# Kernel tuning notes

Hardware: AMD Instinct MI355X
Metric: run time of the kernel (lower is better)

The kernel has to match this reference:

```python
import jax, jax.numpy as jnp
import numpy as np

B, S, HID = 2, 2048, 2048
H, KV, D = 32, 8, 64
GROUPS = H // KV
THETA = 10000.0
SCALE = D ** -0.5
NEG = -1e9


def setup_inputs() -> dict:
    key = jax.random.key(0)
    ks = jax.random.split(key, 5)
    x = jax.random.normal(ks[0], (B, S, 2 * HID), dtype=jnp.float32)
    # Linear weights stored as [in, out] (torch stores [out, in]; y = x @ W.T there)
    Wq = jax.random.normal(ks[1], (2 * HID, H * D), dtype=jnp.float32) * 0.02
    Wk = jax.random.normal(ks[2], (2 * HID, KV * D), dtype=jnp.float32) * 0.02
    Wv = jax.random.normal(ks[3], (2 * HID, KV * D), dtype=jnp.float32) * 0.02
    Wo = jax.random.normal(ks[4], (H * D, HID), dtype=jnp.float32) * 0.02
    # additive causal mask, broadcastable to [B, 1, S, S]
    causal = jnp.tril(jnp.ones((S, S), dtype=bool))
    attention_mask = jnp.where(causal, 0.0, NEG)[None, None].astype(jnp.float32)
    position_ids = jnp.broadcast_to(jnp.arange(S, dtype=jnp.int32)[None, :], (B, S))
    return {"combined_states": x, "attention_mask": attention_mask,
            "position_ids": position_ids, "Wq": Wq, "Wk": Wk, "Wv": Wv, "Wo": Wo}


def _rotate_half(x):
    x1, x2 = jnp.split(x, 2, axis=-1)
    return jnp.concatenate([-x2, x1], axis=-1)


def _rope_cos_sin(position_ids, dtype):
    inv_freq = 1.0 / (THETA ** (jnp.arange(0, D, 2, dtype=jnp.float32) / D))  # [D/2]
    freqs = position_ids.astype(jnp.float32)[..., None] * inv_freq  # [B, S, D/2]
    emb = jnp.concatenate([freqs, freqs], axis=-1)  # [B, S, D]
    return jnp.cos(emb).astype(dtype), jnp.sin(emb).astype(dtype)


def reference(combined_states, attention_mask, position_ids, Wq, Wk, Wv, Wo):
    x = combined_states
    q = (x @ Wq).reshape(B, S, H, D).transpose(0, 2, 1, 3)    # [B, H, S, D]
    k = (x @ Wk).reshape(B, S, KV, D).transpose(0, 2, 1, 3)   # [B, KV, S, D]
    v = (x @ Wv).reshape(B, S, KV, D).transpose(0, 2, 1, 3)
    cos, sin = _rope_cos_sin(position_ids, x.dtype)           # [B, S, D]
    cos, sin = cos[:, None], sin[:, None]                     # [B, 1, S, D]
    q = q * cos + _rotate_half(q) * sin
    k = k * cos + _rotate_half(k) * sin
    k = jnp.repeat(k, GROUPS, axis=1)                         # [B, H, S, D]
    v = jnp.repeat(v, GROUPS, axis=1)
    scores = jnp.einsum('bhqd,bhkd->bhqk', q, k) * SCALE + attention_mask
    probs = jax.nn.softmax(scores.astype(jnp.float32), axis=-1).astype(q.dtype)
    attn = jnp.einsum('bhqk,bhkd->bhqd', probs, v)            # [B, H, S, D]
    attn = attn.transpose(0, 2, 1, 3).reshape(B, S, H * D)
    return attn @ Wo
```

## Files before the change

kernel.cpp:

```cpp
#include <hip/hip_runtime.h>

#define S_LEN 2048
#define BATCH 2
#define HEADS 32
#define KVH   8
#define DH    64

typedef unsigned short u16;
typedef u16   u16x8 __attribute__((ext_vector_type(8)));
typedef u16   u16x4 __attribute__((ext_vector_type(4)));
typedef short s16x8 __attribute__((ext_vector_type(8)));
typedef float f32x4 __attribute__((ext_vector_type(4)));

__device__ __forceinline__ u16 f2bf(float f) {
    unsigned x; __builtin_memcpy(&x, &f, 4);
    x += 0x7fffu + ((x >> 16) & 1u);
    return (u16)(x >> 16);
}
__device__ __forceinline__ u16 f2bf_trunc(float f) {
    unsigned x; __builtin_memcpy(&x, &f, 4);
    return (u16)(x >> 16);
}
__device__ __forceinline__ float bf2f(u16 u) {
    unsigned x = ((unsigned)u) << 16; float f; __builtin_memcpy(&f, &x, 4); return f;
}
__device__ __forceinline__ float fexp2(float x) {
#if __has_builtin(__builtin_amdgcn_exp2f)
    return __builtin_amdgcn_exp2f(x);
#else
    return exp2f(x);
#endif
}
__device__ __forceinline__ void gll16(const void* g, void* l) {
    __builtin_amdgcn_global_load_lds((const __attribute__((address_space(1))) unsigned*)g,
                                     (__attribute__((address_space(3))) unsigned*)l, 16, 0, 0);
}

__global__ __launch_bounds__(256) void k_f32_to_bf16(const float* __restrict__ src,
                                                     u16* __restrict__ dst, int n4) {
    int i = blockIdx.x * 256 + threadIdx.x;
    if (i < n4) {
        f32x4 v = ((const f32x4*)src)[i];
        u16x4 o;
        o.x = f2bf(v.x); o.y = f2bf(v.y); o.z = f2bf(v.z); o.w = f2bf(v.w);
        ((u16x4*)dst)[i] = o;
    }
}

__global__ __launch_bounds__(256) void k_transpose_bf16(const float* __restrict__ src,
                                                        u16* __restrict__ dst,
                                                        int srcCols, int dstStride, int dstRowOff) {
    __shared__ float t[32][33];
    int r0 = blockIdx.x * 32, c0 = blockIdx.y * 32;
    int tx = threadIdx.x & 31, ty = threadIdx.x >> 5;
#pragma unroll
    for (int i = 0; i < 4; ++i)
        t[ty + 8 * i][tx] = src[(size_t)(r0 + ty + 8 * i) * srcCols + (c0 + tx)];
    __syncthreads();
#pragma unroll
    for (int i = 0; i < 4; ++i)
        dst[(size_t)(dstRowOff + c0 + ty + 8 * i) * dstStride + (r0 + tx)] = f2bf(t[tx][ty + 8 * i]);
}

template <int OUT_BF16>
__global__ __launch_bounds__(256) void k_gemm_bt(const u16* __restrict__ A,
                                                 const u16* __restrict__ Bt,
                                                 void* __restrict__ Cout,
                                                 int M, int N, int K) {
    __shared__ __align__(16) u16 As[8192];
    __shared__ __align__(16) u16 Bs[8192];
    int tid = threadIdx.x;
    int wave = tid >> 6, lane = tid & 63, m15 = lane & 15, quad = lane >> 4;
    int wm = (wave >> 1) * 64, wn = (wave & 1) * 64;
    int m0 = blockIdx.y * 128, n0 = blockIdx.x * 128;

    f32x4 acc[4][4];
#pragma unroll
    for (int i = 0; i < 4; ++i)
#pragma unroll
        for (int j = 0; j < 4; ++j) acc[i][j] = (f32x4){0.f, 0.f, 0.f, 0.f};

    int rl8 = lane >> 3;
    int sg8 = ((lane & 7) ^ rl8) * 8;
    const u16* Ag = A  + (size_t)(m0 + wave * 32 + rl8) * K + sg8;
    const u16* Bg = Bt + (size_t)(n0 + wave * 32 + rl8) * K + sg8;
    u16* Asl = As + (wave * 32) * 64;
    u16* Bsl = Bs + (wave * 32) * 64;
    int swq = m15 & 7;

    for (int k0 = 0; k0 < K; k0 += 64) {
        __syncthreads();
#pragma unroll
        for (int i = 0; i < 4; ++i) {
            gll16(Ag + (size_t)(8 * i) * K, Asl + (8 * i) * 64);
            gll16(Bg + (size_t)(8 * i) * K, Bsl + (8 * i) * 64);
        }
        Ag += 64; Bg += 64;
        __syncthreads();

#pragma unroll
        for (int kk = 0; kk < 2; ++kk) {
            int sgr = ((kk * 4 + quad) ^ swq) * 8;
            s16x8 af[4], bfr[4];
#pragma unroll
            for (int mt = 0; mt < 4; ++mt)
                af[mt] = *(const s16x8*)&As[(wm + mt * 16 + m15) * 64 + sgr];
#pragma unroll
            for (int nt = 0; nt < 4; ++nt)
                bfr[nt] = *(const s16x8*)&Bs[(wn + nt * 16 + m15) * 64 + sgr];
#pragma unroll
            for (int mt = 0; mt < 4; ++mt)
#pragma unroll
                for (int nt = 0; nt < 4; ++nt)
                    acc[mt][nt] = __builtin_amdgcn_mfma_f32_16x16x32_bf16(af[mt], bfr[nt], acc[mt][nt], 0, 0, 0);
        }
    }

#pragma unroll
    for (int mt = 0; mt < 4; ++mt)
#pragma unroll
        for (int nt = 0; nt < 4; ++nt)
#pragma unroll
            for (int r = 0; r < 4; ++r) {
                size_t row = m0 + wm + mt * 16 + quad * 4 + r;
                size_t col = n0 + wn + nt * 16 + m15;
                float v = acc[mt][nt][r];
                if (OUT_BF16) ((u16*)Cout)[row * N + col] = f2bf(v);
                else          ((float*)Cout)[row * N + col] = v;
            }
}

__global__ __launch_bounds__(256) void k_vtrans(const u16* __restrict__ qkv, u16* __restrict__ vt) {
    __shared__ u16 t[64][72];
    int s0 = blockIdx.x * 64;
    int bkv = blockIdx.y;
    int tid = threadIdx.x;
    int row = tid >> 2, seg = tid & 3;
    int b = bkv >> 3, kv = bkv & 7;
    const u16* src = qkv + (size_t)(b * S_LEN + s0 + row) * 3072 + 2560 + kv * 64 + seg * 16;
    *(u16x8*)&t[row][seg * 16]     = *(const u16x8*)(src);
    *(u16x8*)&t[row][seg * 16 + 8] = *(const u16x8*)(src + 8);
    __syncthreads();
    int d = tid >> 2, sseg = tid & 3;
    u16x8 o0, o1;
#pragma unroll
    for (int j = 0; j < 8; ++j) { o0[j] = t[sseg * 16 + j][d]; o1[j] = t[sseg * 16 + 8 + j][d]; }
    u16* dst = vt + ((size_t)bkv * 64 + d) * S_LEN + s0 + sseg * 16;
    *(u16x8*)(dst)     = o0;
    *(u16x8*)(dst + 8) = o1;
}

__global__ __launch_bounds__(256) void k_rope(const u16* __restrict__ qkv,
                                              const int* __restrict__ pos_ids,
                                              u16* __restrict__ qo, u16* __restrict__ ko) {
    int bs = blockIdx.x;
    int b = bs >> 11, s = bs & 2047;
    int tid = threadIdx.x;
    float pos = (float)pos_ids[bs];
    const u16* row = qkv + (size_t)bs * 3072;

#pragma unroll
    for (int p = tid; p < 1024; p += 256) {
        int h = p >> 5, i = p & 31;
        float inv = fexp2((float)i * -0.4152410119f);
        float ang = pos * inv;
        float sn, c; __sincosf(ang, &sn, &c);
        float a = bf2f(row[h * 64 + i]);
        float bq = bf2f(row[h * 64 + i + 32]);
        size_t base = ((size_t)(b * HEADS + h) * S_LEN + s) * DH;
        qo[base + i]      = f2bf(a * c - bq * sn);
        qo[base + i + 32] = f2bf(bq * c + a * sn);
    }
    {
        int p = tid;
        if (p < 256) {
            int kv = p >> 5, i = p & 31;
            float inv = fexp2((float)i * -0.4152410119f);
            float ang = pos * inv;
            float sn, c; __sincosf(ang, &sn, &c);
            float a = bf2f(row[2048 + kv * 64 + i]);
            float bk = bf2f(row[2048 + kv * 64 + i + 32]);
            size_t base = ((size_t)(b * KVH + kv) * S_LEN + s) * DH;
            ko[base + i]      = f2bf(a * c - bk * sn);
            ko[base + i + 32] = f2bf(bk * c + a * sn);
        }
    }
}

__global__ __launch_bounds__(256) void k_attn(const u16* __restrict__ q, const u16* __restrict__ k,
                                              const u16* __restrict__ vt, u16* __restrict__ out) {
    __shared__ __align__(16) u16 Qs[4096];
    __shared__ __align__(16) u16 Ks[4096];
    __shared__ __align__(16) u16 Vts[4096];
    __shared__ __align__(16) u16 Ps[4 * 16 * 72];
    int bh = blockIdx.y;
    int b = bh >> 5, h = bh & 31, kvh = h >> 2;
    int tid = threadIdx.x, wave = tid >> 6, lane = tid & 63, m15 = lane & 15, quad = lane >> 4;

    const u16* qhb = q + (size_t)(b * HEADS + h) * S_LEN * DH;
    const u16* kb  = k + (size_t)(b * KVH + kvh) * S_LEN * DH;
    const u16* vb  = vt + (size_t)(b * KVH + kvh) * DH * S_LEN;
    u16* PsW = &Ps[wave * 16 * 72];
    const float C = 0.1803368801f;

    int rl8 = lane >> 3;
    int sg8 = ((lane & 7) ^ rl8) * 8;
    int swq = m15 & 7;

    for (int half = 0; half < 2; ++half) {
        int jt = half ? (31 - (int)blockIdx.x) : (int)blockIdx.x;
        int q0 = jt * 64;
        __syncthreads();
        {
            const u16* qg = qhb + (size_t)(q0 + wave * 16 + rl8) * DH + sg8;
            gll16(qg,          Qs + (wave * 16) * 64);
            gll16(qg + 8 * DH, Qs + (wave * 16 + 8) * 64);
        }

        float lsum[4];
        f32x4 oacc[4];
#pragma unroll
        for (int r = 0; r < 4; ++r) lsum[r] = 0.f;
#pragma unroll
        for (int dt = 0; dt < 4; ++dt) oacc[dt] = (f32x4){0.f, 0.f, 0.f, 0.f};

        for (int ib = 0; ib <= jt; ++ib) {
            int kk0 = ib * 64;
            __syncthreads();
            {
                const u16* kg = kb + (size_t)(kk0 + wave * 16 + rl8) * DH + sg8;
                gll16(kg,          Ks + (wave * 16) * 64);
                gll16(kg + 8 * DH, Ks + (wave * 16 + 8) * 64);
                const u16* vg = vb + (size_t)(wave * 16 + rl8) * S_LEN + kk0 + sg8;
                gll16(vg,             Vts + (wave * 16) * 64);
                gll16(vg + 8 * S_LEN, Vts + (wave * 16 + 8) * 64);
            }
            __syncthreads();

            f32x4 sacc[4];
#pragma unroll
            for (int nt = 0; nt < 4; ++nt) sacc[nt] = (f32x4){0.f, 0.f, 0.f, 0.f};
#pragma unroll
            for (int kk = 0; kk < 2; ++kk) {
                int sgr = ((kk * 4 + quad) ^ swq) * 8;
                s16x8 aF = *(const s16x8*)&Qs[(wave * 16 + m15) * 64 + sgr];
#pragma unroll
                for (int nt = 0; nt < 4; ++nt) {
                    s16x8 bF = *(const s16x8*)&Ks[(nt * 16 + m15) * 64 + sgr];
                    sacc[nt] = __builtin_amdgcn_mfma_f32_16x16x32_bf16(aF, bF, sacc[nt], 0, 0, 0);
                }
            }

            bool diag = (ib == jt);
#pragma unroll
            for (int r = 0; r < 4; ++r) {
                int qrow = q0 + wave * 16 + quad * 4 + r;
#pragma unroll
                for (int nt = 0; nt < 4; ++nt) {
                    float s2 = sacc[nt][r] * C - 12.0f;
                    if (diag && (kk0 + nt * 16 + m15 > qrow)) s2 = -1e30f;
                    float p = fexp2(s2);
                    lsum[r] += p;
                    PsW[(quad * 4 + r) * 72 + nt * 16 + m15] = f2bf_trunc(p);
                }
            }

#pragma unroll
            for (int kk = 0; kk < 2; ++kk) {
                s16x8 aF = *(const s16x8*)&PsW[m15 * 72 + kk * 32 + quad * 8];
                int sgr = ((kk * 4 + quad) ^ swq) * 8;
#pragma unroll
                for (int dt = 0; dt < 4; ++dt) {
                    s16x8 bF = *(const s16x8*)&Vts[(dt * 16 + m15) * 64 + sgr];
                    oacc[dt] = __builtin_amdgcn_mfma_f32_16x16x32_bf16(aF, bF, oacc[dt], 0, 0, 0);
                }
            }
        }

#pragma unroll
        for (int r = 0; r < 4; ++r) {
            float ls = lsum[r];
#pragma unroll
            for (int off = 1; off < 16; off <<= 1) ls += __shfl_xor(ls, off, 64);
            float inv = 1.f / ls;
            int qrow = q0 + wave * 16 + quad * 4 + r;
#pragma unroll
            for (int dt = 0; dt < 4; ++dt)
                out[((size_t)(b * S_LEN) + qrow) * (size_t)(HEADS * DH) + h * DH + dt * 16 + m15] =
                    f2bf(oacc[dt][r] * inv);
        }
    }
}

extern "C" void kernel_launch(void* const* d_in, const int* in_sizes, int n_in,
                              void* d_out, int out_size, void* d_ws, size_t ws_size,
                              hipStream_t stream) {
    const float* x  = (const float*)d_in[0];
    const int*   pos = (const int*)d_in[2];
    const float* Wq = (const float*)d_in[3];
    const float* Wk = (const float*)d_in[4];
    const float* Wv = (const float*)d_in[5];
    const float* Wo = (const float*)d_in[6];

    char* ws = (char*)d_ws;
    const size_t NEED = 92274688;
    if (ws_size < NEED) return;

    u16* xbf   = (u16*)(ws);
    u16* vt    = (u16*)(ws + 16777216);
    u16* wqkvt = (u16*)(ws + 33554432);
    u16* wot   = (u16*)(ws + 58720256);
    u16* qkv   = (u16*)(ws + 67108864);
    u16* qro   = wqkvt;
    u16* kro   = qro + 8388608;
    u16* attn  = xbf;

    k_f32_to_bf16<<<16384, 256, 0, stream>>>(x, xbf, 4194304);
    {
        dim3 gq(128, 64); k_transpose_bf16<<<gq, 256, 0, stream>>>(Wq, wqkvt, 2048, 4096, 0);
        dim3 gk(128, 16); k_transpose_bf16<<<gk, 256, 0, stream>>>(Wk, wqkvt, 512, 4096, 2048);
        k_transpose_bf16<<<gk, 256, 0, stream>>>(Wv, wqkvt, 512, 4096, 2560);
        dim3 go(64, 64);  k_transpose_bf16<<<go, 256, 0, stream>>>(Wo, wot, 2048, 2048, 0);
    }
    { dim3 g(24, 32); k_gemm_bt<1><<<g, 256, 0, stream>>>(xbf, wqkvt, qkv, 4096, 3072, 4096); }
    { dim3 g(32, 16); k_vtrans<<<g, 256, 0, stream>>>(qkv, vt); }
    k_rope<<<4096, 256, 0, stream>>>(qkv, pos, qro, kro);
    { dim3 g(16, 64); k_attn<<<g, 256, 0, stream>>>(qro, kro, vt, attn); }
    { dim3 g(16, 32); k_gemm_bt<0><<<g, 256, 0, stream>>>(attn, wot, (float*)d_out, 4096, 2048, 2048); }
}
```

Before: 426.9 us.

## Process two KV tiles per attention barrier, merge weight transposes, permute V layout

The attention kernel now loads 128 keys and V columns per barrier pair and runs two 64-key sub-tiles between syncs, which halves barrier and load-issue overhead per key. P is packed into 8-byte LDS writes, and the V-transpose kernel permutes its key order so the packed P layout lines up with V. The four weight-transpose launches are merged into one kernel. The trade-off is double the K/V shared memory, which may lower occupancy, and coupled permutations of the P and V layouts that must agree for the result to be correct.

Result: faster. 410.9 us (-3.7%).

```diff
diff --git a/kernel.cpp b/kernel.cpp
--- a/kernel.cpp
+++ b/kernel.cpp
@@ -7,18 +7,16 @@
 #define DH    64
 
 typedef unsigned short u16;
+typedef unsigned int   u32;
 typedef u16   u16x8 __attribute__((ext_vector_type(8)));
 typedef u16   u16x4 __attribute__((ext_vector_type(4)));
 typedef short s16x8 __attribute__((ext_vector_type(8)));
 typedef float f32x4 __attribute__((ext_vector_type(4)));
+typedef u32   u32x2 __attribute__((ext_vector_type(2)));
 
 __device__ __forceinline__ u16 f2bf(float f) {
     unsigned x; __builtin_memcpy(&x, &f, 4);
     x += 0x7fffu + ((x >> 16) & 1u);
-    return (u16)(x >> 16);
-}
-__device__ __forceinline__ u16 f2bf_trunc(float f) {
-    unsigned x; __builtin_memcpy(&x, &f, 4);
     return (u16)(x >> 16);
 }
 __device__ __forceinline__ float bf2f(u16 u) {
@@ -47,11 +45,17 @@
     }
 }
 
-__global__ __launch_bounds__(256) void k_transpose_bf16(const float* __restrict__ src,
-                                                        u16* __restrict__ dst,
-                                                        int srcCols, int dstStride, int dstRowOff) {
+__global__ __launch_bounds__(256) void k_wprep(const float* __restrict__ Wq, const float* __restrict__ Wk,
+                                               const float* __restrict__ Wv, const float* __restrict__ Wo,
+                                               u16* __restrict__ wqkvt, u16* __restrict__ wot) {
     __shared__ float t[32][33];
-    int r0 = blockIdx.x * 32, c0 = blockIdx.y * 32;
+    int id = blockIdx.x;
+    const float* src; u16* dst; int srcCols, dstStride, dstRowOff, bx, by;
+    if (id < 8192)       { src = Wq; dst = wqkvt; srcCols = 2048; dstStride = 4096; dstRowOff = 0;    bx = id & 127; by = id >> 7; }
+    else if (id < 10240) { id -= 8192;  src = Wk; dst = wqkvt; srcCols = 512; dstStride = 4096; dstRowOff = 2048; bx = id & 127; by = id >> 7; }
+    else if (id < 12288) { id -= 10240; src = Wv; dst = wqkvt; srcCols = 512; dstStride = 4096; dstRowOff = 2560; bx = id & 127; by = id >> 7; }
+    else                 { id -= 12288; src = Wo; dst = wot;   srcCols = 2048; dstStride = 2048; dstRowOff = 0;   bx = id & 63;  by = id >> 6; }
+    int r0 = bx * 32, c0 = by * 32;
     int tx = threadIdx.x & 31, ty = threadIdx.x >> 5;
 #pragma unroll
     for (int i = 0; i < 4; ++i)
@@ -144,7 +148,10 @@
     int d = tid >> 2, sseg = tid & 3;
     u16x8 o0, o1;
 #pragma unroll
-    for (int j = 0; j < 8; ++j) { o0[j] = t[sseg * 16 + j][d]; o1[j] = t[sseg * 16 + 8 + j][d]; }
+    for (int j = 0; j < 8; ++j) {
+        o0[j] = t[(j & 3) * 16 + sseg * 4 + (j >> 2)][d];
+        o1[j] = t[(j & 3) * 16 + sseg * 4 + (j >> 2) + 2][d];
+    }
     u16* dst = vt + ((size_t)bkv * 64 + d) * S_LEN + s0 + sseg * 16;
     *(u16x8*)(dst)     = o0;
     *(u16x8*)(dst + 8) = o1;
@@ -190,8 +197,8 @@
 __global__ __launch_bounds__(256) void k_attn(const u16* __restrict__ q, const u16* __restrict__ k,
                                               const u16* __restrict__ vt, u16* __restrict__ out) {
     __shared__ __align__(16) u16 Qs[4096];
-    __shared__ __align__(16) u16 Ks[4096];
-    __shared__ __align__(16) u16 Vts[4096];
+    __shared__ __align__(16) u16 Ks[8192];
+    __shared__ __align__(16) u16 Vts[8192];
     __shared__ __align__(16) u16 Ps[4 * 16 * 72];
     int bh = blockIdx.y;
     int b = bh >> 5, h = bh & 31, kvh = h >> 2;
@@ -206,6 +213,8 @@
     int rl8 = lane >> 3;
     int sg8 = ((lane & 7) ^ rl8) * 8;
     int swq = m15 & 7;
+    int vrow = lane >> 4;
+    int vgrp = lane & 15;
 
     for (int half = 0; half < 2; ++half) {
         int jt = half ? (31 - (int)blockIdx.x) : (int)blockIdx.x;
@@ -224,55 +233,69 @@
 #pragma unroll
         for (int dt = 0; dt < 4; ++dt) oacc[dt] = (f32x4){0.f, 0.f, 0.f, 0.f};
 
-        for (int ib = 0; ib <= jt; ++ib) {
+        for (int ib = 0; ib <= jt; ib += 2) {
             int kk0 = ib * 64;
+            int nsub = (jt - ib >= 1) ? 2 : 1;
             __syncthreads();
             {
-                const u16* kg = kb + (size_t)(kk0 + wave * 16 + rl8) * DH + sg8;
-                gll16(kg,          Ks + (wave * 16) * 64);
-                gll16(kg + 8 * DH, Ks + (wave * 16 + 8) * 64);
-                const u16* vg = vb + (size_t)(wave * 16 + rl8) * S_LEN + kk0 + sg8;
-                gll16(vg,             Vts + (wave * 16) * 64);
-                gll16(vg + 8 * S_LEN, Vts + (wave * 16 + 8) * 64);
+                const u16* kg = kb + (size_t)(kk0 + wave * 32 + rl8) * DH + sg8;
+#pragma unroll
+                for (int i = 0; i < 4; ++i)
+                    gll16(kg + (size_t)(8 * i) * DH, Ks + (wave * 32 + 8 * i) * 64);
+#pragma unroll
+                for (int i = 0; i < 4; ++i) {
+                    int d = wave * 16 + 4 * i + vrow;
+                    const u16* vg = vb + (size_t)d * S_LEN + kk0 + ((vgrp ^ (d & 7)) * 8);
+                    gll16(vg, Vts + (wave * 16 + 4 * i) * 128);
+                }
             }
             __syncthreads();
 
-            f32x4 sacc[4];
-#pragma unroll
-            for (int nt = 0; nt < 4; ++nt) sacc[nt] = (f32x4){0.f, 0.f, 0.f, 0.f};
-#pragma unroll
-            for (int kk = 0; kk < 2; ++kk) {
-                int sgr = ((kk * 4 + quad) ^ swq) * 8;
-                s16x8 aF = *(const s16x8*)&Qs[(wave * 16 + m15) * 64 + sgr];
-#pragma unroll
-                for (int nt = 0; nt < 4; ++nt) {
-                    s16x8 bF = *(const s16x8*)&Ks[(nt * 16 + m15) * 64 + sgr];
-                    sacc[nt] = __builtin_amdgcn_mfma_f32_16x16x32_bf16(aF, bF, sacc[nt], 0, 0, 0);
+            for (int sub = 0; sub < nsub; ++sub) {
+                f32x4 sacc[4];
+#pragma unroll
+                for (int nt = 0; nt < 4; ++nt) sacc[nt] = (f32x4){0.f, 0.f, 0.f, 0.f};
+#pragma unroll
+                for (int kk = 0; kk < 2; ++kk) {
+                    int sgr = ((kk * 4 + quad) ^ swq) * 8;
+                    s16x8 aF = *(const s16x8*)&Qs[(wave * 16 + m15) * 64 + sgr];
+#pragma unroll
+                    for (int nt = 0; nt < 4; ++nt) {
+                        s16x8 bF = *(const s16x8*)&Ks[(sub * 64 + nt * 16 + m15) * 64 + sgr];
+                        sacc[nt] = __builtin_amdgcn_mfma_f32_16x16x32_bf16(aF, bF, sacc[nt], 0, 0, 0);
+                    }
                 }
-            }
-
-            bool diag = (ib == jt);
-#pragma unroll
-            for (int r = 0; r < 4; ++r) {
-                int qrow = q0 + wave * 16 + quad * 4 + r;
-#pragma unroll
-                for (int nt = 0; nt < 4; ++nt) {
-                    float s2 = sacc[nt][r] * C - 12.0f;
-                    if (diag && (kk0 + nt * 16 + m15 > qrow)) s2 = -1e30f;
-                    float p = fexp2(s2);
-                    lsum[r] += p;
-                    PsW[(quad * 4 + r) * 72 + nt * 16 + m15] = f2bf_trunc(p);
+
+                bool dsub = (kk0 + sub * 64) == q0;
+#pragma unroll
+                for (int r = 0; r < 4; ++r) {
+                    int qrr = wave * 16 + quad * 4 + r;
+                    float p0[4];
+#pragma unroll
+                    for (int nt = 0; nt < 4; ++nt) {
+                        float s2 = sacc[nt][r] * C - 12.0f;
+                        if (dsub && (nt * 16 + m15 > qrr)) s2 = -1e30f;
+                        p0[nt] = fexp2(s2);
+                        lsum[r] += p0[nt];
+                    }
+                    unsigned a0, a1, a2, a3;
+                    __builtin_memcpy(&a0, &p0[0], 4); __builtin_memcpy(&a1, &p0[1], 4);
+                    __builtin_memcpy(&a2, &p0[2], 4); __builtin_memcpy(&a3, &p0[3], 4);
+                    u32x2 w;
+                    w.x = (a0 >> 16) | (a1 & 0xffff0000u);
+                    w.y = (a2 >> 16) | (a3 & 0xffff0000u);
+                    *(u32x2*)&PsW[(quad * 4 + r) * 72 + m15 * 4] = w;
                 }
-            }
-
-#pragma unroll
-            for (int kk = 0; kk < 2; ++kk) {
-                s16x8 aF = *(const s16x8*)&PsW[m15 * 72 + kk * 32 + quad * 8];
-                int sgr = ((kk * 4 + quad) ^ swq) * 8;
-#pragma unroll
-                for (int dt = 0; dt < 4; ++dt) {
-                    s16x8 bF = *(const s16x8*)&Vts[(dt * 16 + m15) * 64 + sgr];
-                    oacc[dt] = __builtin_amdgcn_mfma_f32_16x16x32_bf16(aF, bF, oacc[dt], 0, 0, 0);
+
+#pragma unroll
+                for (int kk = 0; kk < 2; ++kk) {
+                    s16x8 aF = *(const s16x8*)&PsW[m15 * 72 + kk * 32 + quad * 8];
+                    int g = (sub * 8 + kk * 4 + quad) ^ swq;
+#pragma unroll
+                    for (int dt = 0; dt < 4; ++dt) {
+                        s16x8 bF = *(const s16x8*)&Vts[(dt * 16 + m15) * 128 + g * 8];
+                        oacc[dt] = __builtin_amdgcn_mfma_f32_16x16x32_bf16(aF, bF, oacc[dt], 0, 0, 0);
+                    }
                 }
             }
         }
@@ -316,12 +339,7 @@
     u16* attn  = xbf;
 
     k_f32_to_bf16<<<16384, 256, 0, stream>>>(x, xbf, 4194304);
-    {
-        dim3 gq(128, 64); k_transpose_bf16<<<gq, 256, 0, stream>>>(Wq, wqkvt, 2048, 4096, 0);
-        dim3 gk(128, 16); k_transpose_bf16<<<gk, 256, 0, stream>>>(Wk, wqkvt, 512, 4096, 2048);
-        k_transpose_bf16<<<gk, 256, 0, stream>>>(Wv, wqkvt, 512, 4096, 2560);
-        dim3 go(64, 64);  k_transpose_bf16<<<go, 256, 0, stream>>>(Wo, wot, 2048, 2048, 0);
-    }
+    k_wprep<<<16384, 256, 0, stream>>>(Wq, Wk, Wv, Wo, wqkvt, wot);
     { dim3 g(24, 32); k_gemm_bt<1><<<g, 256, 0, stream>>>(xbf, wqkvt, qkv, 4096, 3072, 4096); }
     { dim3 g(32, 16); k_vtrans<<<g, 256, 0, stream>>>(qkv, vt); }
     k_rope<<<4096, 256, 0, stream>>>(qkv, pos, qro, kro);
```
